# Performance work log

Measured on AMD Instinct MI355X. Metric: run time of the kernel, lower is better.

## Reference

```python
import jax, jax.numpy as jnp
import numpy as np

N_EDGES = 250000
N_ATOMS = 10000
K_L = [256, 192, 128, 64]  # n_element_channels(32) * n_max_l [8,6,4,2]
L_MAX = 3


def setup_inputs() -> dict:
    key = jax.random.key(0)
    ks = jax.random.split(key, 16)
    inp = {}
    for l in range(L_MAX + 1):
        inp[f"sh_{l}"] = jax.random.normal(ks[l], (N_EDGES, 2 * l + 1, 1), dtype=jnp.float32)
        inp[f"rb_{l}"] = jax.random.normal(ks[4 + l], (N_EDGES, K_L[l]), dtype=jnp.float32)
    inp["emb"] = jax.random.normal(ks[8], (N_ATOMS, 1, K_L[0]), dtype=jnp.float32)
    inp["centers"] = jax.random.randint(ks[9], (N_EDGES,), 0, N_ATOMS, dtype=jnp.int32)
    inp["neighbors"] = jax.random.randint(ks[10], (N_EDGES,), 0, N_ATOMS, dtype=jnp.int32)
    return inp


def reference(sh_0, sh_1, sh_2, sh_3, rb_0, rb_1, rb_2, rb_3, emb, centers, neighbors):
    """Per-l: gather neighbor embeddings, 3-way elementwise multiply with
    spherical harmonics and radial basis, scatter-add into per-center density."""
    shs = [sh_0, sh_1, sh_2, sh_3]
    rbs = [rb_0, rb_1, rb_2, rb_3]
    emb_n = emb[neighbors]  # [E, 1, k_max0] -- gathered once, sliced per l
    outs = []
    for l in range(L_MAX + 1):
        k_l = rbs[l].shape[1]
        # [E, 2l+1, 1] * [E, 1, k_l] * [E, 1, k_l] -> [E, 2l+1, k_l]
        msg = shs[l] * rbs[l][:, None, :] * emb_n[:, :, :k_l]
        dens = jax.ops.segment_sum(msg, centers, num_segments=N_ATOMS)
        outs.append(dens)  # [n_atoms, 2l+1, k_l]
    return tuple(outs)
```

## Files before the change

kernel.cpp:

```cpp
#include <hip/hip_runtime.h>

#define N_EDGES 250000
#define N_ATOMS 10000


__global__ void zero_counts_kernel(int* __restrict__ counts) {
    int i = blockIdx.x * blockDim.x + threadIdx.x;
    if (i < N_ATOMS) counts[i] = 0;
}

__global__ void count_edges_kernel(const int* __restrict__ centers,
                                   int* __restrict__ counts) {
    int e = blockIdx.x * blockDim.x + threadIdx.x;
    if (e < N_EDGES) atomicAdd(&counts[centers[e]], 1);
}

__global__ void scan_offsets_kernel(const int* __restrict__ counts,
                                    int* __restrict__ offsets,
                                    int* __restrict__ cursor) {
    __shared__ int sdata[256];
    const int t = threadIdx.x;
    const int CH = 40;
    const int base = t * CH;
    int sum = 0;
    for (int i = 0; i < CH; ++i) {
        int idx = base + i;
        if (idx < N_ATOMS) sum += counts[idx];
    }
    sdata[t] = sum;
    __syncthreads();
    for (int off = 1; off < 256; off <<= 1) {
        int v = (t >= off) ? sdata[t - off] : 0;
        __syncthreads();
        sdata[t] += v;
        __syncthreads();
    }
    int incl = sdata[t];
    int run = incl - sum;
    for (int i = 0; i < CH; ++i) {
        int idx = base + i;
        if (idx < N_ATOMS) {
            offsets[idx] = run;
            cursor[idx] = run;
            run += counts[idx];
        }
    }
    if (t == 255) offsets[N_ATOMS] = incl;
}

__global__ void fill_list_kernel(const int* __restrict__ centers,
                                 int* __restrict__ cursor,
                                 int* __restrict__ elist) {
    int e = blockIdx.x * blockDim.x + threadIdx.x;
    if (e < N_EDGES) {
        int p = atomicAdd(&cursor[centers[e]], 1);
        elist[p] = e;
    }
}


__global__ __launch_bounds__(256) void density_kernel(
    const float* __restrict__ sh0, const float* __restrict__ sh1,
    const float* __restrict__ sh2, const float* __restrict__ sh3,
    const float* __restrict__ rb0, const float* __restrict__ rb1,
    const float* __restrict__ rb2, const float* __restrict__ rb3,
    const float* __restrict__ emb, const int* __restrict__ neighbors,
    const int* __restrict__ offsets, const int* __restrict__ elist,
    float* __restrict__ out) {
    const int wave = threadIdx.x >> 6;
    const int a = blockIdx.x * 4 + wave;
    const int t = threadIdx.x & 63;

    const int s = offsets[a];
    const int e = offsets[a + 1];

    float a0[4] = {0.f, 0.f, 0.f, 0.f};
    float a1[3][3] = {};
    float a2[5][2] = {};
    float a3[7] = {};

    for (int i = s; i < e; ++i) {
        const int eg = elist[i];
        const int nb = neighbors[eg];

        const float* er = emb + (size_t)nb * 256;
        const float em0 = er[t];
        const float em1 = er[t + 64];
        const float em2 = er[t + 128];
        const float em3 = er[t + 192];

        const float* r0 = rb0 + (size_t)eg * 256;
        const float* r1 = rb1 + (size_t)eg * 192;
        const float* r2 = rb2 + (size_t)eg * 128;
        const float* r3 = rb3 + (size_t)eg * 64;

        const float p00 = r0[t] * em0;
        const float p01 = r0[t + 64] * em1;
        const float p02 = r0[t + 128] * em2;
        const float p03 = r0[t + 192] * em3;
        const float p10 = r1[t] * em0;
        const float p11 = r1[t + 64] * em1;
        const float p12 = r1[t + 128] * em2;
        const float p20 = r2[t] * em0;
        const float p21 = r2[t + 64] * em1;
        const float p30 = r3[t] * em0;

        const float s0 = sh0[eg];
        a0[0] += s0 * p00;
        a0[1] += s0 * p01;
        a0[2] += s0 * p02;
        a0[3] += s0 * p03;

        const float* s1 = sh1 + (size_t)eg * 3;
#pragma unroll
        for (int m = 0; m < 3; ++m) {
            const float sm = s1[m];
            a1[m][0] += sm * p10;
            a1[m][1] += sm * p11;
            a1[m][2] += sm * p12;
        }
        const float* s2 = sh2 + (size_t)eg * 5;
#pragma unroll
        for (int m = 0; m < 5; ++m) {
            const float sm = s2[m];
            a2[m][0] += sm * p20;
            a2[m][1] += sm * p21;
        }
        const float* s3 = sh3 + (size_t)eg * 7;
#pragma unroll
        for (int m = 0; m < 7; ++m) {
            a3[m] += s3[m] * p30;
        }
    }

    const size_t O1 = (size_t)N_ATOMS * 256;
    const size_t O2 = O1 + (size_t)N_ATOMS * 3 * 192;
    const size_t O3 = O2 + (size_t)N_ATOMS * 5 * 128;

    float* o0 = out + (size_t)a * 256;
#pragma unroll
    for (int j = 0; j < 4; ++j) o0[t + 64 * j] = a0[j];

    float* o1 = out + O1 + (size_t)a * 3 * 192;
#pragma unroll
    for (int m = 0; m < 3; ++m)
#pragma unroll
        for (int j = 0; j < 3; ++j) o1[m * 192 + t + 64 * j] = a1[m][j];

    float* o2 = out + O2 + (size_t)a * 5 * 128;
#pragma unroll
    for (int m = 0; m < 5; ++m)
#pragma unroll
        for (int j = 0; j < 2; ++j) o2[m * 128 + t + 64 * j] = a2[m][j];

    float* o3 = out + O3 + (size_t)a * 7 * 64;
#pragma unroll
    for (int m = 0; m < 7; ++m) o3[m * 64 + t] = a3[m];
}


extern "C" void kernel_launch(void* const* d_in, const int* in_sizes, int n_in,
                              void* d_out, int out_size, void* d_ws, size_t ws_size,
                              hipStream_t stream) {
    const float* sh0 = (const float*)d_in[0];
    const float* rb0 = (const float*)d_in[1];
    const float* sh1 = (const float*)d_in[2];
    const float* rb1 = (const float*)d_in[3];
    const float* sh2 = (const float*)d_in[4];
    const float* rb2 = (const float*)d_in[5];
    const float* sh3 = (const float*)d_in[6];
    const float* rb3 = (const float*)d_in[7];
    const float* emb = (const float*)d_in[8];
    const int* centers = (const int*)d_in[9];
    const int* neighbors = (const int*)d_in[10];
    float* out = (float*)d_out;

    int* counts = (int*)d_ws;
    int* offsets = counts + N_ATOMS;
    int* cursor = offsets + (N_ATOMS + 1);
    int* elist = cursor + N_ATOMS;

    zero_counts_kernel<<<(N_ATOMS + 255) / 256, 256, 0, stream>>>(counts);
    count_edges_kernel<<<(N_EDGES + 255) / 256, 256, 0, stream>>>(centers, counts);
    scan_offsets_kernel<<<1, 256, 0, stream>>>(counts, offsets, cursor);
    fill_list_kernel<<<(N_EDGES + 255) / 256, 256, 0, stream>>>(centers, cursor, elist);
    density_kernel<<<N_ATOMS / 4, 256, 0, stream>>>(
        sh0, sh1, sh2, sh3, rb0, rb1, rb2, rb3, emb, neighbors, offsets, elist,
        out);
}
```

Before: 798.7 us.

## Split per-atom edges across two waves and pre-pack sorted SH coefficients

The fill-list pass now stores an (edge, neighbor) pair and writes all 16 spherical-harmonic coefficients for each edge into a contiguous float4 block in center-sorted order. The density kernel assigns two waves to each atom, each handling alternating edges, and combines the two partial sums through shared memory before writing. It also makes the edge and SH values wave-uniform with readfirstlane, and uses float4 loads for rb0 and emb. The aim is to double memory-level parallelism on the latency-bound per-atom edge walk and to remove the dependent neighbor lookup and the scattered SH loads. The cost is an extra 16 MB workspace write, extra work in the fill kernel, and an LDS reduction with a block barrier.

```diff
diff --git a/kernel.cpp b/kernel.cpp
--- a/kernel.cpp
+++ b/kernel.cpp
@@ -2,6 +2,13 @@
 
 #define N_EDGES 250000
 #define N_ATOMS 10000
+
+__device__ __forceinline__ int rfl_i(int x) {
+    return __builtin_amdgcn_readfirstlane(x);
+}
+__device__ __forceinline__ float rfl_f(float x) {
+    return __uint_as_float(__builtin_amdgcn_readfirstlane(__float_as_uint(x)));
+}
 
 
 __global__ void zero_counts_kernel(int* __restrict__ counts) {
@@ -49,113 +56,160 @@
 }
 
 __global__ void fill_list_kernel(const int* __restrict__ centers,
+                                 const int* __restrict__ neighbors,
+                                 const float* __restrict__ sh0,
+                                 const float* __restrict__ sh1,
+                                 const float* __restrict__ sh2,
+                                 const float* __restrict__ sh3,
                                  int* __restrict__ cursor,
-                                 int* __restrict__ elist) {
+                                 int2* __restrict__ elist2,
+                                 float4* __restrict__ shp) {
     int e = blockIdx.x * blockDim.x + threadIdx.x;
-    if (e < N_EDGES) {
-        int p = atomicAdd(&cursor[centers[e]], 1);
-        elist[p] = e;
-    }
+    if (e >= N_EDGES) return;
+    int p = atomicAdd(&cursor[centers[e]], 1);
+    elist2[p] = make_int2(e, neighbors[e]);
+    float4 va, vb, vc, vd;
+    va.x = sh0[e];
+    const float* s1 = sh1 + 3 * (size_t)e;
+    va.y = s1[0]; va.z = s1[1]; va.w = s1[2];
+    const float* s2 = sh2 + 5 * (size_t)e;
+    vb.x = s2[0]; vb.y = s2[1]; vb.z = s2[2]; vb.w = s2[3];
+    vc.x = s2[4];
+    const float* s3 = sh3 + 7 * (size_t)e;
+    vc.y = s3[0]; vc.z = s3[1]; vc.w = s3[2];
+    vd.x = s3[3]; vd.y = s3[4]; vd.z = s3[5]; vd.w = s3[6];
+    float4* o = shp + (size_t)p * 4;
+    o[0] = va; o[1] = vb; o[2] = vc; o[3] = vd;
 }
 
 
 __global__ __launch_bounds__(256) void density_kernel(
-    const float* __restrict__ sh0, const float* __restrict__ sh1,
-    const float* __restrict__ sh2, const float* __restrict__ sh3,
     const float* __restrict__ rb0, const float* __restrict__ rb1,
     const float* __restrict__ rb2, const float* __restrict__ rb3,
-    const float* __restrict__ emb, const int* __restrict__ neighbors,
-    const int* __restrict__ offsets, const int* __restrict__ elist,
+    const float* __restrict__ emb, const int* __restrict__ offsets,
+    const int2* __restrict__ elist2, const float4* __restrict__ shp,
     float* __restrict__ out) {
+    __shared__ float red[2][1920];
+
     const int wave = threadIdx.x >> 6;
-    const int a = blockIdx.x * 4 + wave;
+    const int pairidx = wave >> 1;
+    const int sub = wave & 1;
+    const int a = blockIdx.x * 2 + pairidx;
     const int t = threadIdx.x & 63;
 
-    const int s = offsets[a];
-    const int e = offsets[a + 1];
-
-    float a0[4] = {0.f, 0.f, 0.f, 0.f};
+    const int s = rfl_i(offsets[a]);
+    const int e = rfl_i(offsets[a + 1]);
+
+    float4 a0 = {0.f, 0.f, 0.f, 0.f};
     float a1[3][3] = {};
     float a2[5][2] = {};
     float a3[7] = {};
 
-    for (int i = s; i < e; ++i) {
-        const int eg = elist[i];
-        const int nb = neighbors[eg];
-
-        const float* er = emb + (size_t)nb * 256;
-        const float em0 = er[t];
-        const float em1 = er[t + 64];
-        const float em2 = er[t + 128];
-        const float em3 = er[t + 192];
-
-        const float* r0 = rb0 + (size_t)eg * 256;
-        const float* r1 = rb1 + (size_t)eg * 192;
-        const float* r2 = rb2 + (size_t)eg * 128;
-        const float* r3 = rb3 + (size_t)eg * 64;
-
-        const float p00 = r0[t] * em0;
-        const float p01 = r0[t + 64] * em1;
-        const float p02 = r0[t + 128] * em2;
-        const float p03 = r0[t + 192] * em3;
-        const float p10 = r1[t] * em0;
-        const float p11 = r1[t + 64] * em1;
-        const float p12 = r1[t + 128] * em2;
-        const float p20 = r2[t] * em0;
-        const float p21 = r2[t + 64] * em1;
-        const float p30 = r3[t] * em0;
-
-        const float s0 = sh0[eg];
-        a0[0] += s0 * p00;
-        a0[1] += s0 * p01;
-        a0[2] += s0 * p02;
-        a0[3] += s0 * p03;
-
-        const float* s1 = sh1 + (size_t)eg * 3;
+    for (int i = s + sub; i < e; i += 2) {
+        const int2 en = elist2[i];
+        const int eg = rfl_i(en.x);
+        const int nb = rfl_i(en.y);
+
+        const float4 sv0 = shp[(size_t)i * 4 + 0];
+        const float4 sv1 = shp[(size_t)i * 4 + 1];
+        const float4 sv2 = shp[(size_t)i * 4 + 2];
+        const float4 sv3 = shp[(size_t)i * 4 + 3];
+
+        const float* er = emb + ((size_t)nb << 8);
+        const float4 em4 = *(const float4*)(er + 4 * t);
+        const float emA = er[t];
+        const float emB = er[t + 64];
+        const float emC = er[t + 128];
+
+        const float4 r04 = *(const float4*)(rb0 + ((size_t)eg << 8) + 4 * t);
+        const float* r1p = rb1 + (size_t)eg * 192;
+        const float r1A = r1p[t], r1B = r1p[t + 64], r1C = r1p[t + 128];
+        const float* r2p = rb2 + ((size_t)eg << 7);
+        const float r2A = r2p[t], r2B = r2p[t + 64];
+        const float r3A = rb3[((size_t)eg << 6) + t];
+
+        const float p0x = r04.x * em4.x, p0y = r04.y * em4.y;
+        const float p0z = r04.z * em4.z, p0w = r04.w * em4.w;
+        const float pA = r1A * emA, pB = r1B * emB, pC = r1C * emC;
+        const float qA = r2A * emA, qB = r2B * emB;
+        const float v3 = r3A * emA;
+
+        const float s0 = rfl_f(sv0.x);
+        a0.x += s0 * p0x; a0.y += s0 * p0y; a0.z += s0 * p0z; a0.w += s0 * p0w;
+
+        const float sh1v[3] = {rfl_f(sv0.y), rfl_f(sv0.z), rfl_f(sv0.w)};
 #pragma unroll
         for (int m = 0; m < 3; ++m) {
-            const float sm = s1[m];
-            a1[m][0] += sm * p10;
-            a1[m][1] += sm * p11;
-            a1[m][2] += sm * p12;
+            a1[m][0] += sh1v[m] * pA;
+            a1[m][1] += sh1v[m] * pB;
+            a1[m][2] += sh1v[m] * pC;
         }
-        const float* s2 = sh2 + (size_t)eg * 5;
+        const float sh2v[5] = {rfl_f(sv1.x), rfl_f(sv1.y), rfl_f(sv1.z),
+                               rfl_f(sv1.w), rfl_f(sv2.x)};
 #pragma unroll
         for (int m = 0; m < 5; ++m) {
-            const float sm = s2[m];
-            a2[m][0] += sm * p20;
-            a2[m][1] += sm * p21;
+            a2[m][0] += sh2v[m] * qA;
+            a2[m][1] += sh2v[m] * qB;
         }
-        const float* s3 = sh3 + (size_t)eg * 7;
-#pragma unroll
-        for (int m = 0; m < 7; ++m) {
-            a3[m] += s3[m] * p30;
-        }
-    }
-
-    const size_t O1 = (size_t)N_ATOMS * 256;
-    const size_t O2 = O1 + (size_t)N_ATOMS * 3 * 192;
-    const size_t O3 = O2 + (size_t)N_ATOMS * 5 * 128;
-
-    float* o0 = out + (size_t)a * 256;
-#pragma unroll
-    for (int j = 0; j < 4; ++j) o0[t + 64 * j] = a0[j];
-
-    float* o1 = out + O1 + (size_t)a * 3 * 192;
-#pragma unroll
-    for (int m = 0; m < 3; ++m)
-#pragma unroll
-        for (int j = 0; j < 3; ++j) o1[m * 192 + t + 64 * j] = a1[m][j];
-
-    float* o2 = out + O2 + (size_t)a * 5 * 128;
-#pragma unroll
-    for (int m = 0; m < 5; ++m)
-#pragma unroll
-        for (int j = 0; j < 2; ++j) o2[m * 128 + t + 64 * j] = a2[m][j];
-
-    float* o3 = out + O3 + (size_t)a * 7 * 64;
-#pragma unroll
-    for (int m = 0; m < 7; ++m) o3[m * 64 + t] = a3[m];
+        const float sh3v[7] = {rfl_f(sv2.y), rfl_f(sv2.z), rfl_f(sv2.w),
+                               rfl_f(sv3.x), rfl_f(sv3.y), rfl_f(sv3.z),
+                               rfl_f(sv3.w)};
+#pragma unroll
+        for (int m = 0; m < 7; ++m) a3[m] += sh3v[m] * v3;
+    }
+
+    float* R = red[pairidx];
+    if (sub == 1) {
+        reinterpret_cast<float4*>(R)[t] = a0;
+#pragma unroll
+        for (int m = 0; m < 3; ++m)
+#pragma unroll
+            for (int j = 0; j < 3; ++j) R[256 + m * 192 + 64 * j + t] = a1[m][j];
+#pragma unroll
+        for (int m = 0; m < 5; ++m)
+#pragma unroll
+            for (int j = 0; j < 2; ++j) R[832 + m * 128 + 64 * j + t] = a2[m][j];
+#pragma unroll
+        for (int m = 0; m < 7; ++m) R[1472 + m * 64 + t] = a3[m];
+    }
+    __syncthreads();
+    if (sub == 0) {
+        const float4 rv = reinterpret_cast<const float4*>(R)[t];
+        a0.x += rv.x; a0.y += rv.y; a0.z += rv.z; a0.w += rv.w;
+#pragma unroll
+        for (int m = 0; m < 3; ++m)
+#pragma unroll
+            for (int j = 0; j < 3; ++j) a1[m][j] += R[256 + m * 192 + 64 * j + t];
+#pragma unroll
+        for (int m = 0; m < 5; ++m)
+#pragma unroll
+            for (int j = 0; j < 2; ++j) a2[m][j] += R[832 + m * 128 + 64 * j + t];
+#pragma unroll
+        for (int m = 0; m < 7; ++m) a3[m] += R[1472 + m * 64 + t];
+
+        const size_t O1 = (size_t)N_ATOMS * 256;
+        const size_t O2 = O1 + (size_t)N_ATOMS * 3 * 192;
+        const size_t O3 = O2 + (size_t)N_ATOMS * 5 * 128;
+
+        float* o0 = out + (size_t)a * 256;
+        reinterpret_cast<float4*>(o0)[t] = a0;
+
+        float* o1 = out + O1 + (size_t)a * 3 * 192;
+#pragma unroll
+        for (int m = 0; m < 3; ++m)
+#pragma unroll
+            for (int j = 0; j < 3; ++j) o1[m * 192 + 64 * j + t] = a1[m][j];
+
+        float* o2 = out + O2 + (size_t)a * 5 * 128;
+#pragma unroll
+        for (int m = 0; m < 5; ++m)
+#pragma unroll
+            for (int j = 0; j < 2; ++j) o2[m * 128 + 64 * j + t] = a2[m][j];
+
+        float* o3 = out + O3 + (size_t)a * 7 * 64;
+#pragma unroll
+        for (int m = 0; m < 7; ++m) o3[m * 64 + t] = a3[m];
+    }
 }
 
 
@@ -175,16 +229,17 @@
     const int* neighbors = (const int*)d_in[10];
     float* out = (float*)d_out;
 
-    int* counts = (int*)d_ws;
+    float4* shp = (float4*)d_ws;
+    int2* elist2 = (int2*)((char*)d_ws + 16000000);
+    int* counts = (int*)((char*)d_ws + 18000000);
     int* offsets = counts + N_ATOMS;
     int* cursor = offsets + (N_ATOMS + 1);
-    int* elist = cursor + N_ATOMS;
 
     zero_counts_kernel<<<(N_ATOMS + 255) / 256, 256, 0, stream>>>(counts);
     count_edges_kernel<<<(N_EDGES + 255) / 256, 256, 0, stream>>>(centers, counts);
     scan_offsets_kernel<<<1, 256, 0, stream>>>(counts, offsets, cursor);
-    fill_list_kernel<<<(N_EDGES + 255) / 256, 256, 0, stream>>>(centers, cursor, elist);
-    density_kernel<<<N_ATOMS / 4, 256, 0, stream>>>(
-        sh0, sh1, sh2, sh3, rb0, rb1, rb2, rb3, emb, neighbors, offsets, elist,
-        out);
-}
+    fill_list_kernel<<<(N_EDGES + 255) / 256, 256, 0, stream>>>(
+        centers, neighbors, sh0, sh1, sh2, sh3, cursor, elist2, shp);
+    density_kernel<<<N_ATOMS / 2, 256, 0, stream>>>(
+        rb0, rb1, rb2, rb3, emb, offsets, elist2, shp, out);
+}
```

Result: faster. 717.4 us (-10.2%).
